# Optimization experiments

Measured on AMD Instinct MI355X. Metric: run time of the kernel, lower is better.

The kernel has to match this reference:

```python
import jax, jax.numpy as jnp
import numpy as np

# CIN config: input_dim (num_fields) = 32, cross_layer_sizes = [128, 128, 128], split_half = True
NUM_FIELDS = 32
EMBED_DIM = 16
BATCH = 4096
CROSS_SIZES = [128, 128, 128]


def setup_inputs() -> dict:
    key = jax.random.key(0)
    ks = jax.random.split(key, 8)
    x = jax.random.normal(ks[0], (BATCH, NUM_FIELDS, EMBED_DIM), dtype=jnp.float32)
    # Conv1d(kernel_size=1) weights: (out_ch, in_ch) + bias (out_ch,)
    prev = NUM_FIELDS
    inp = {"x": x}
    for i, cs in enumerate(CROSS_SIZES):
        in_ch = NUM_FIELDS * prev
        scale = 1.0 / np.sqrt(in_ch)
        inp[f"W{i}"] = jax.random.uniform(ks[1 + 2 * i], (cs, in_ch), dtype=jnp.float32, minval=-scale, maxval=scale)
        inp[f"b{i}"] = jax.random.uniform(ks[2 + 2 * i], (cs,), dtype=jnp.float32, minval=-scale, maxval=scale)
        prev = cs // 2  # split_half (applied after all but last, but prev for next conv uses halved size)
    return inp


def _cin_forward(x, Ws, bs):
    # x: (B, F, E)
    x0 = x
    h = x
    xs = []
    n_layers = len(Ws)
    for i in range(n_layers):
        B, F, E = x0.shape
        G = h.shape[1]
        # outer product over field dims -> (B, F*G, E)
        z = (x0[:, :, None, :] * h[:, None, :, :]).reshape(B, F * G, E)
        # 1x1 conv == channel matmul; bias broadcast over embed dim; relu
        y = jax.nn.relu(jnp.einsum('oc,bce->boe', Ws[i], z) + bs[i][None, :, None])
        if i != n_layers - 1:
            half = y.shape[1] // 2
            x_keep, h = y[:, :half, :], y[:, half:, :]
        else:
            x_keep, h = y, y
        xs.append(x_keep)
    return jnp.sum(jnp.concatenate(xs, axis=1), axis=2)  # (B, fc_input_dim)


def reference(x, W0, b0, W1, b1, W2, b2):
    return _cin_forward(x, [W0, W1, W2], [b0, b1, b2])
```

## Files before the change

kernel.cpp:

```cpp
#include <hip/hip_runtime.h>

typedef _Float16 half_t;
typedef _Float16 v8h __attribute__((ext_vector_type(8)));
typedef float v4f __attribute__((ext_vector_type(4)));

#define XTP 40

typedef __attribute__((address_space(3))) unsigned int lds_u32;
typedef const __attribute__((address_space(1))) unsigned int glb_u32;

__device__ __forceinline__ void dma16(const half_t* g, half_t* l, int lane) {
  __builtin_amdgcn_global_load_lds((glb_u32*)(g + lane * 8), (lds_u32*)(l), 16, 0, 0);
}

#define WAITVM(N) __builtin_amdgcn_s_waitcnt(0xF70 | (N))
#define SCHED0()  __builtin_amdgcn_sched_barrier(0)

__global__ __launch_bounds__(256) void prep_x(const float* __restrict__ x, half_t* __restrict__ xt) {
  __shared__ half_t t[8 * 512];
  const int tid = threadIdx.x;
  const size_t b0 = (size_t)blockIdx.x * 8;
#pragma unroll
  for (int i = 0; i < 4; ++i) {
    int idx = (i * 256 + tid) * 4;
    float4 v = *(const float4*)(x + b0 * 512 + idx);
    int e = idx & 15, f = (idx >> 4) & 31, b = idx >> 9;
    half_t* d = t + b * 512 + f;
    d[(e + 0) * 32] = (half_t)v.x;
    d[(e + 1) * 32] = (half_t)v.y;
    d[(e + 2) * 32] = (half_t)v.z;
    d[(e + 3) * 32] = (half_t)v.w;
  }
  __syncthreads();
#pragma unroll
  for (int i = 0; i < 2; ++i) {
    int c = i * 256 + tid;
    *(uint4*)(xt + b0 * 512 + c * 8) = *(const uint4*)(t + c * 8);
  }
}

__global__ __launch_bounds__(256) void prep_w(const float* __restrict__ src, half_t* __restrict__ dst,
                                              int ktot, int nchunk) {
  int i = blockIdx.x * 256 + threadIdx.x;
  if (i >= nchunk) return;
  int o = i & 127, k8 = i >> 7;
  const float* s = src + (size_t)o * ktot + k8 * 8;
  float4 f0 = *(const float4*)s;
  float4 f1 = *(const float4*)(s + 4);
  union { half_t h[8]; uint4 u; } pk;
  pk.h[0] = (half_t)f0.x; pk.h[1] = (half_t)f0.y; pk.h[2] = (half_t)f0.z; pk.h[3] = (half_t)f0.w;
  pk.h[4] = (half_t)f1.x; pk.h[5] = (half_t)f1.y; pk.h[6] = (half_t)f1.z; pk.h[7] = (half_t)f1.w;
  *(uint4*)(dst + (size_t)i * 8) = pk.u;
}

template <int G, int KTOT, int KEEP, int OUT_BASE, bool H_OUT, bool H_IS_X>
__global__ __launch_bounds__(512, 1) void cin_layer(const half_t* __restrict__ xt,
                                                    const half_t* __restrict__ hin,
                                                    const half_t* __restrict__ wgt,
                                                    const float* __restrict__ bias,
                                                    half_t* __restrict__ hout,
                                                    float* __restrict__ out) {
  constexpr int NS = KTOT / 32;
  constexpr int SPO = (G == 64) ? 16 : 8;
  constexpr int NOCT = NS / SPO;
  constexpr int NSEL = (G == 64) ? 2 : 1;
  __shared__ __align__(16) half_t xt_lds[256 * XTP];
  __shared__ __align__(16) half_t w_lds[4 * 4096];
  __shared__ float bias_lds[128];

  const int tid = threadIdx.x;
  const int lane = tid & 63;
  const int wv = tid >> 6;
  const size_t b0 = (size_t)blockIdx.x * 16;
  const int phase = (blockIdx.x >> 3) & 3;

  {
    const int r = tid >> 1, c = (tid & 1) * 16;
    const half_t* src = xt + b0 * 512 + r * 32 + c;
    uint4 q0 = *(const uint4*)(src);
    uint4 q1 = *(const uint4*)(src + 8);
    *(uint4*)(xt_lds + r * XTP + c) = q0;
    *(uint4*)(xt_lds + r * XTP + c + 8) = q1;
  }
  if (tid < 128) bias_lds[tid] = bias[tid];

  const int wm = (wv & 1) * 64;
  const int wb = (wv >> 1) * 4;
  const int col = lane & 15;
  const int kq = lane >> 4;

  int lrow[4];
#pragma unroll
  for (int ni = 0; ni < 4; ++ni) lrow[ni] = (wb + ni) * 16 + col;

  v8h hreg[4][NSEL];
  if (!H_IS_X) {
#pragma unroll
    for (int ni = 0; ni < 4; ++ni) {
      const half_t* hp = hin + ((b0 + wb + ni) * 16 + col) * 64 + kq * 8;
      hreg[ni][0] = *(const v8h*)(hp);
      if (NSEL > 1) hreg[ni][NSEL - 1] = *(const v8h*)(hp + 32);
    }
  }

#pragma unroll
  for (int p = 0; p < 3; ++p) {
    const half_t* wsrc = wgt + (size_t)(phase * SPO + p) * 4096;
    half_t* pb = w_lds + p * 4096;
    dma16(wsrc + wv * 512, pb + wv * 512, lane);
  }

  __syncthreads();

  if (H_IS_X) {
#pragma unroll
    for (int ni = 0; ni < 4; ++ni)
      hreg[ni][0] = *(const v8h*)(xt_lds + lrow[ni] * XTP + kq * 8);
  }

  v4f acc[4][4] = {};

#pragma unroll 1
  for (int oi = 0; oi < NOCT - 1; ++oi) {
    const int oct_a = (oi + phase) & 3;
    const int next_a = (oi + 1 + phase) & 3;
    v8h xv[4];
#pragma unroll
    for (int ni = 0; ni < 4; ++ni)
      xv[ni] = *(const v8h*)(xt_lds + lrow[ni] * XTP + oct_a * 8);
#pragma unroll
    for (int t = 0; t < SPO; ++t) {
      SCHED0(); WAITVM(2); __builtin_amdgcn_s_barrier(); SCHED0();
      {
        const int tp = t + 3;
        const half_t* wsrc = (tp < SPO)
            ? wgt + (size_t)(oct_a * SPO + tp) * 4096
            : wgt + (size_t)(next_a * SPO + (tp - SPO)) * 4096;
        half_t* pb = w_lds + (tp & 3) * 4096;
        dma16(wsrc + wv * 512, pb + wv * 512, lane);
      }
      const half_t* rb = w_lds + (t & 3) * 4096;
      const int j = (G == 64) ? (t >> 1) : t;
      const int sel = (G == 64) ? (t & 1) : 0;
      v8h a[4], bfr[4];
#pragma unroll
      for (int mi = 0; mi < 4; ++mi)
        a[mi] = *(const v8h*)(rb + (kq * 128 + wm + mi * 16 + col) * 8);
#pragma unroll
      for (int ni = 0; ni < 4; ++ni)
        bfr[ni] = hreg[ni][sel] * xv[ni][j];
#pragma unroll
      for (int mi = 0; mi < 4; ++mi)
#pragma unroll
        for (int ni = 0; ni < 4; ++ni)
          acc[mi][ni] = __builtin_amdgcn_mfma_f32_16x16x32_f16(a[mi], bfr[ni], acc[mi][ni], 0, 0, 0);
    }
  }

  {
    const int oct_a = (NOCT - 1 + phase) & 3;
    v8h xv[4];
#pragma unroll
    for (int ni = 0; ni < 4; ++ni)
      xv[ni] = *(const v8h*)(xt_lds + lrow[ni] * XTP + oct_a * 8);
#pragma unroll
    for (int t = 0; t < SPO; ++t) {
      SCHED0();
      if (t < SPO - 2) { WAITVM(2); } else if (t == SPO - 2) { WAITVM(1); } else { WAITVM(0); }
      __builtin_amdgcn_s_barrier(); SCHED0();
      if (t + 3 < SPO) {
        const int tp = t + 3;
        const half_t* wsrc = wgt + (size_t)(oct_a * SPO + tp) * 4096;
        half_t* pb = w_lds + (tp & 3) * 4096;
        dma16(wsrc + wv * 512, pb + wv * 512, lane);
      }
      const half_t* rb = w_lds + (t & 3) * 4096;
      const int j = (G == 64) ? (t >> 1) : t;
      const int sel = (G == 64) ? (t & 1) : 0;
      v8h a[4], bfr[4];
#pragma unroll
      for (int mi = 0; mi < 4; ++mi)
        a[mi] = *(const v8h*)(rb + (kq * 128 + wm + mi * 16 + col) * 8);
#pragma unroll
      for (int ni = 0; ni < 4; ++ni)
        bfr[ni] = hreg[ni][sel] * xv[ni][j];
#pragma unroll
      for (int mi = 0; mi < 4; ++mi)
#pragma unroll
        for (int ni = 0; ni < 4; ++ni)
          acc[mi][ni] = __builtin_amdgcn_mfma_f32_16x16x32_f16(a[mi], bfr[ni], acc[mi][ni], 0, 0, 0);
    }
  }

#pragma unroll
  for (int mi = 0; mi < 4; ++mi) {
    const int o_base = wm + mi * 16 + kq * 4;
#pragma unroll
    for (int ni = 0; ni < 4; ++ni) {
      const int bb = wb + ni;
      float v[4];
#pragma unroll
      for (int r = 0; r < 4; ++r)
        v[r] = fmaxf(acc[mi][ni][r] + bias_lds[o_base + r], 0.0f);
      if (H_OUT && o_base >= 64) {
        union { half_t h[4]; uint2 u; } pk;
#pragma unroll
        for (int r = 0; r < 4; ++r) pk.h[r] = (half_t)v[r];
        *(uint2*)(hout + ((b0 + bb) * 16 + col) * 64 + (o_base - 64)) = pk.u;
      }
      if (o_base < KEEP) {
#pragma unroll
        for (int r = 0; r < 4; ++r) {
          float sv = v[r];
          sv += __shfl_xor(sv, 1);
          sv += __shfl_xor(sv, 2);
          sv += __shfl_xor(sv, 4);
          sv += __shfl_xor(sv, 8);
          if (col == 0) out[(b0 + bb) * 256 + OUT_BASE + o_base + r] = sv;
        }
      }
    }
  }
}

extern "C" void kernel_launch(void* const* d_in, const int* in_sizes, int n_in,
                              void* d_out, int out_size, void* d_ws, size_t ws_size,
                              hipStream_t stream) {
  const float* x  = (const float*)d_in[0];
  const float* W0 = (const float*)d_in[1];
  const float* b0 = (const float*)d_in[2];
  const float* W1 = (const float*)d_in[3];
  const float* b1 = (const float*)d_in[4];
  const float* W2 = (const float*)d_in[5];
  const float* b2 = (const float*)d_in[6];
  float* out = (float*)d_out;
  char* ws = (char*)d_ws;

  half_t* xt  = (half_t*)(ws);
  half_t* w0h = (half_t*)(ws + (4u << 20));
  half_t* w1h = (half_t*)(ws + (4u << 20) + (256u << 10));
  half_t* w2h = (half_t*)(ws + (4u << 20) + (768u << 10));
  half_t* h1  = (half_t*)(ws + (4u << 20) + (1280u << 10));
  half_t* h2  = (half_t*)(ws + (12u << 20) + (1280u << 10));

  prep_x<<<512, 256, 0, stream>>>(x, xt);
  prep_w<<<64, 256, 0, stream>>>(W0, w0h, 1024, 16384);
  prep_w<<<128, 256, 0, stream>>>(W1, w1h, 2048, 32768);
  prep_w<<<128, 256, 0, stream>>>(W2, w2h, 2048, 32768);

  cin_layer<32, 1024, 64, 0, true, true><<<256, 512, 0, stream>>>(xt, xt, w0h, b0, h1, out);
  cin_layer<64, 2048, 64, 64, true, false><<<256, 512, 0, stream>>>(xt, h1, w1h, b1, h2, out);
  cin_layer<64, 2048, 128, 128, false, false><<<256, 512, 0, stream>>>(xt, h2, w2h, b2, nullptr, out);
}
```

Measured before the change: 178.5 us.

## Fuse input prep and all three CIN layers into one kernel with LDS-resident h

Replaces the separate prep_x kernel and three per-layer kernels with a single fused kernel. It converts x to fp16 directly into LDS, keeps the intermediate h activations in LDS between layers, and reads bias straight from global memory. The batch tile per block is halved to 8 rows with 512 blocks, and the three weight-conversion launches are merged into one. This removes the global round-trips for xt, h1 and h2 and several launches. In exchange, each block streams the full weight set, so total weight traffic doubles, and each barrier step now issues half as many MFMAs.

After: 148.7 us. 16.7% less time.

```diff
diff --git a/kernel.cpp b/kernel.cpp
--- a/kernel.cpp
+++ b/kernel.cpp
@@ -5,6 +5,7 @@
 typedef float v4f __attribute__((ext_vector_type(4)));
 
 #define XTP 40
+#define HP  72
 
 typedef __attribute__((address_space(3))) unsigned int lds_u32;
 typedef const __attribute__((address_space(1))) unsigned int glb_u32;
@@ -16,117 +17,77 @@
 #define WAITVM(N) __builtin_amdgcn_s_waitcnt(0xF70 | (N))
 #define SCHED0()  __builtin_amdgcn_sched_barrier(0)
 
-__global__ __launch_bounds__(256) void prep_x(const float* __restrict__ x, half_t* __restrict__ xt) {
-  __shared__ half_t t[8 * 512];
-  const int tid = threadIdx.x;
-  const size_t b0 = (size_t)blockIdx.x * 8;
-#pragma unroll
-  for (int i = 0; i < 4; ++i) {
-    int idx = (i * 256 + tid) * 4;
-    float4 v = *(const float4*)(x + b0 * 512 + idx);
-    int e = idx & 15, f = (idx >> 4) & 31, b = idx >> 9;
-    half_t* d = t + b * 512 + f;
-    d[(e + 0) * 32] = (half_t)v.x;
-    d[(e + 1) * 32] = (half_t)v.y;
-    d[(e + 2) * 32] = (half_t)v.z;
-    d[(e + 3) * 32] = (half_t)v.w;
-  }
-  __syncthreads();
-#pragma unroll
-  for (int i = 0; i < 2; ++i) {
-    int c = i * 256 + tid;
-    *(uint4*)(xt + b0 * 512 + c * 8) = *(const uint4*)(t + c * 8);
-  }
-}
-
-__global__ __launch_bounds__(256) void prep_w(const float* __restrict__ src, half_t* __restrict__ dst,
-                                              int ktot, int nchunk) {
+__global__ __launch_bounds__(256) void prep_w_all(const float* __restrict__ W0,
+                                                  const float* __restrict__ W1,
+                                                  const float* __restrict__ W2,
+                                                  half_t* __restrict__ w0h,
+                                                  half_t* __restrict__ w1h,
+                                                  half_t* __restrict__ w2h) {
   int i = blockIdx.x * 256 + threadIdx.x;
-  if (i >= nchunk) return;
-  int o = i & 127, k8 = i >> 7;
+  const float* src; half_t* dst; int ktot; int j;
+  if (i < 16384)      { src = W0; dst = w0h; ktot = 1024; j = i; }
+  else if (i < 49152) { src = W1; dst = w1h; ktot = 2048; j = i - 16384; }
+  else                { src = W2; dst = w2h; ktot = 2048; j = i - 49152; }
+  int o = j & 127, k8 = j >> 7;
   const float* s = src + (size_t)o * ktot + k8 * 8;
   float4 f0 = *(const float4*)s;
   float4 f1 = *(const float4*)(s + 4);
   union { half_t h[8]; uint4 u; } pk;
   pk.h[0] = (half_t)f0.x; pk.h[1] = (half_t)f0.y; pk.h[2] = (half_t)f0.z; pk.h[3] = (half_t)f0.w;
   pk.h[4] = (half_t)f1.x; pk.h[5] = (half_t)f1.y; pk.h[6] = (half_t)f1.z; pk.h[7] = (half_t)f1.w;
-  *(uint4*)(dst + (size_t)i * 8) = pk.u;
+  *(uint4*)(dst + (size_t)j * 8) = pk.u;
 }
 
 template <int G, int KTOT, int KEEP, int OUT_BASE, bool H_OUT, bool H_IS_X>
-__global__ __launch_bounds__(512, 1) void cin_layer(const half_t* __restrict__ xt,
-                                                    const half_t* __restrict__ hin,
-                                                    const half_t* __restrict__ wgt,
-                                                    const float* __restrict__ bias,
-                                                    half_t* __restrict__ hout,
-                                                    float* __restrict__ out) {
-  constexpr int NS = KTOT / 32;
+__device__ __forceinline__ void layer(const half_t* __restrict__ wgt,
+                                      const float* __restrict__ bias,
+                                      half_t* __restrict__ xt_lds,
+                                      half_t* __restrict__ h_lds,
+                                      half_t* __restrict__ w_ring,
+                                      float* __restrict__ out,
+                                      size_t b0, int tid, int phase) {
   constexpr int SPO = (G == 64) ? 16 : 8;
-  constexpr int NOCT = NS / SPO;
+  constexpr int NOCT = (KTOT / 32) / SPO;
   constexpr int NSEL = (G == 64) ? 2 : 1;
-  __shared__ __align__(16) half_t xt_lds[256 * XTP];
-  __shared__ __align__(16) half_t w_lds[4 * 4096];
-  __shared__ float bias_lds[128];
-
-  const int tid = threadIdx.x;
   const int lane = tid & 63;
   const int wv = tid >> 6;
-  const size_t b0 = (size_t)blockIdx.x * 16;
-  const int phase = (blockIdx.x >> 3) & 3;
-
-  {
-    const int r = tid >> 1, c = (tid & 1) * 16;
-    const half_t* src = xt + b0 * 512 + r * 32 + c;
-    uint4 q0 = *(const uint4*)(src);
-    uint4 q1 = *(const uint4*)(src + 8);
-    *(uint4*)(xt_lds + r * XTP + c) = q0;
-    *(uint4*)(xt_lds + r * XTP + c + 8) = q1;
-  }
-  if (tid < 128) bias_lds[tid] = bias[tid];
-
   const int wm = (wv & 1) * 64;
-  const int wb = (wv >> 1) * 4;
+  const int wb = (wv >> 1) * 2;
   const int col = lane & 15;
   const int kq = lane >> 4;
 
-  int lrow[4];
-#pragma unroll
-  for (int ni = 0; ni < 4; ++ni) lrow[ni] = (wb + ni) * 16 + col;
-
-  v8h hreg[4][NSEL];
-  if (!H_IS_X) {
-#pragma unroll
-    for (int ni = 0; ni < 4; ++ni) {
-      const half_t* hp = hin + ((b0 + wb + ni) * 16 + col) * 64 + kq * 8;
-      hreg[ni][0] = *(const v8h*)(hp);
-      if (NSEL > 1) hreg[ni][NSEL - 1] = *(const v8h*)(hp + 32);
-    }
+  int lrow[2];
+#pragma unroll
+  for (int ni = 0; ni < 2; ++ni) lrow[ni] = (wb + ni) * 16 + col;
+
+  __syncthreads();
+
+  const half_t* hb = H_IS_X ? xt_lds : h_lds;
+  const int hpitch = H_IS_X ? XTP : HP;
+  v8h hreg[2][NSEL];
+#pragma unroll
+  for (int ni = 0; ni < 2; ++ni) {
+    const half_t* hp = hb + lrow[ni] * hpitch + kq * 8;
+    hreg[ni][0] = *(const v8h*)hp;
+    if (NSEL > 1) hreg[ni][NSEL - 1] = *(const v8h*)(hp + 32);
   }
 
 #pragma unroll
   for (int p = 0; p < 3; ++p) {
     const half_t* wsrc = wgt + (size_t)(phase * SPO + p) * 4096;
-    half_t* pb = w_lds + p * 4096;
-    dma16(wsrc + wv * 512, pb + wv * 512, lane);
-  }
-
+    dma16(wsrc + wv * 512, w_ring + p * 4096 + wv * 512, lane);
+  }
   __syncthreads();
 
-  if (H_IS_X) {
-#pragma unroll
-    for (int ni = 0; ni < 4; ++ni)
-      hreg[ni][0] = *(const v8h*)(xt_lds + lrow[ni] * XTP + kq * 8);
-  }
-
-  v4f acc[4][4] = {};
+  v4f acc[4][2] = {};
 
 #pragma unroll 1
   for (int oi = 0; oi < NOCT - 1; ++oi) {
     const int oct_a = (oi + phase) & 3;
     const int next_a = (oi + 1 + phase) & 3;
-    v8h xv[4];
-#pragma unroll
-    for (int ni = 0; ni < 4; ++ni)
+    v8h xv[2];
+#pragma unroll
+    for (int ni = 0; ni < 2; ++ni)
       xv[ni] = *(const v8h*)(xt_lds + lrow[ni] * XTP + oct_a * 8);
 #pragma unroll
     for (int t = 0; t < SPO; ++t) {
@@ -136,32 +97,31 @@
         const half_t* wsrc = (tp < SPO)
             ? wgt + (size_t)(oct_a * SPO + tp) * 4096
             : wgt + (size_t)(next_a * SPO + (tp - SPO)) * 4096;
-        half_t* pb = w_lds + (tp & 3) * 4096;
-        dma16(wsrc + wv * 512, pb + wv * 512, lane);
-      }
-      const half_t* rb = w_lds + (t & 3) * 4096;
+        dma16(wsrc + wv * 512, w_ring + (tp & 3) * 4096 + wv * 512, lane);
+      }
+      const half_t* rb = w_ring + (t & 3) * 4096;
       const int j = (G == 64) ? (t >> 1) : t;
       const int sel = (G == 64) ? (t & 1) : 0;
-      v8h a[4], bfr[4];
+      v8h a[4], bfr[2];
 #pragma unroll
       for (int mi = 0; mi < 4; ++mi)
         a[mi] = *(const v8h*)(rb + (kq * 128 + wm + mi * 16 + col) * 8);
 #pragma unroll
-      for (int ni = 0; ni < 4; ++ni)
+      for (int ni = 0; ni < 2; ++ni)
         bfr[ni] = hreg[ni][sel] * xv[ni][j];
 #pragma unroll
       for (int mi = 0; mi < 4; ++mi)
 #pragma unroll
-        for (int ni = 0; ni < 4; ++ni)
+        for (int ni = 0; ni < 2; ++ni)
           acc[mi][ni] = __builtin_amdgcn_mfma_f32_16x16x32_f16(a[mi], bfr[ni], acc[mi][ni], 0, 0, 0);
     }
   }
 
   {
     const int oct_a = (NOCT - 1 + phase) & 3;
-    v8h xv[4];
-#pragma unroll
-    for (int ni = 0; ni < 4; ++ni)
+    v8h xv[2];
+#pragma unroll
+    for (int ni = 0; ni < 2; ++ni)
       xv[ni] = *(const v8h*)(xt_lds + lrow[ni] * XTP + oct_a * 8);
 #pragma unroll
     for (int t = 0; t < SPO; ++t) {
@@ -171,23 +131,22 @@
       if (t + 3 < SPO) {
         const int tp = t + 3;
         const half_t* wsrc = wgt + (size_t)(oct_a * SPO + tp) * 4096;
-        half_t* pb = w_lds + (tp & 3) * 4096;
-        dma16(wsrc + wv * 512, pb + wv * 512, lane);
-      }
-      const half_t* rb = w_lds + (t & 3) * 4096;
+        dma16(wsrc + wv * 512, w_ring + (tp & 3) * 4096 + wv * 512, lane);
+      }
+      const half_t* rb = w_ring + (t & 3) * 4096;
       const int j = (G == 64) ? (t >> 1) : t;
       const int sel = (G == 64) ? (t & 1) : 0;
-      v8h a[4], bfr[4];
+      v8h a[4], bfr[2];
 #pragma unroll
       for (int mi = 0; mi < 4; ++mi)
         a[mi] = *(const v8h*)(rb + (kq * 128 + wm + mi * 16 + col) * 8);
 #pragma unroll
-      for (int ni = 0; ni < 4; ++ni)
+      for (int ni = 0; ni < 2; ++ni)
         bfr[ni] = hreg[ni][sel] * xv[ni][j];
 #pragma unroll
       for (int mi = 0; mi < 4; ++mi)
 #pragma unroll
-        for (int ni = 0; ni < 4; ++ni)
+        for (int ni = 0; ni < 2; ++ni)
           acc[mi][ni] = __builtin_amdgcn_mfma_f32_16x16x32_f16(a[mi], bfr[ni], acc[mi][ni], 0, 0, 0);
     }
   }
@@ -195,18 +154,19 @@
 #pragma unroll
   for (int mi = 0; mi < 4; ++mi) {
     const int o_base = wm + mi * 16 + kq * 4;
-#pragma unroll
-    for (int ni = 0; ni < 4; ++ni) {
+    float4 b4 = *(const float4*)(bias + o_base);
+#pragma unroll
+    for (int ni = 0; ni < 2; ++ni) {
       const int bb = wb + ni;
       float v[4];
 #pragma unroll
       for (int r = 0; r < 4; ++r)
-        v[r] = fmaxf(acc[mi][ni][r] + bias_lds[o_base + r], 0.0f);
+        v[r] = fmaxf(acc[mi][ni][r] + (&b4.x)[r], 0.0f);
       if (H_OUT && o_base >= 64) {
         union { half_t h[4]; uint2 u; } pk;
 #pragma unroll
         for (int r = 0; r < 4; ++r) pk.h[r] = (half_t)v[r];
-        *(uint2*)(hout + ((b0 + bb) * 16 + col) * 64 + (o_base - 64)) = pk.u;
+        *(uint2*)(h_lds + (bb * 16 + col) * HP + (o_base - 64)) = pk.u;
       }
       if (o_base < KEEP) {
 #pragma unroll
@@ -221,6 +181,39 @@
       }
     }
   }
+}
+
+__global__ __launch_bounds__(512, 4) void cin_fused(const float* __restrict__ x,
+                                                    const half_t* __restrict__ w0h,
+                                                    const half_t* __restrict__ w1h,
+                                                    const half_t* __restrict__ w2h,
+                                                    const float* __restrict__ b0p,
+                                                    const float* __restrict__ b1p,
+                                                    const float* __restrict__ b2p,
+                                                    float* __restrict__ out) {
+  __shared__ __align__(16) half_t xt_lds[128 * XTP];
+  __shared__ __align__(16) half_t h_lds[128 * HP];
+  __shared__ __align__(16) half_t w_ring[4 * 4096];
+
+  const int tid = threadIdx.x;
+  const size_t b0 = (size_t)blockIdx.x * 8;
+  const int phase = (blockIdx.x >> 3) & 3;
+
+#pragma unroll
+  for (int i = 0; i < 2; ++i) {
+    int idx = (i * 512 + tid) * 4;
+    float4 v = *(const float4*)(x + b0 * 512 + idx);
+    int e = idx & 15, f = (idx >> 4) & 31, b = idx >> 9;
+    half_t* d = xt_lds + (b * 16 + e) * XTP + f;
+    d[0 * XTP] = (half_t)v.x;
+    d[1 * XTP] = (half_t)v.y;
+    d[2 * XTP] = (half_t)v.z;
+    d[3 * XTP] = (half_t)v.w;
+  }
+
+  layer<32, 1024, 64, 0, true, true>(w0h, b0p, xt_lds, h_lds, w_ring, out, b0, tid, phase);
+  layer<64, 2048, 64, 64, true, false>(w1h, b1p, xt_lds, h_lds, w_ring, out, b0, tid, phase);
+  layer<64, 2048, 128, 128, false, false>(w2h, b2p, xt_lds, h_lds, w_ring, out, b0, tid, phase);
 }
 
 extern "C" void kernel_launch(void* const* d_in, const int* in_sizes, int n_in,
@@ -236,19 +229,10 @@
   float* out = (float*)d_out;
   char* ws = (char*)d_ws;
 
-  half_t* xt  = (half_t*)(ws);
-  half_t* w0h = (half_t*)(ws + (4u << 20));
-  half_t* w1h = (half_t*)(ws + (4u << 20) + (256u << 10));
-  half_t* w2h = (half_t*)(ws + (4u << 20) + (768u << 10));
-  half_t* h1  = (half_t*)(ws + (4u << 20) + (1280u << 10));
-  half_t* h2  = (half_t*)(ws + (12u << 20) + (1280u << 10));
-
-  prep_x<<<512, 256, 0, stream>>>(x, xt);
-  prep_w<<<64, 256, 0, stream>>>(W0, w0h, 1024, 16384);
-  prep_w<<<128, 256, 0, stream>>>(W1, w1h, 2048, 32768);
-  prep_w<<<128, 256, 0, stream>>>(W2, w2h, 2048, 32768);
-
-  cin_layer<32, 1024, 64, 0, true, true><<<256, 512, 0, stream>>>(xt, xt, w0h, b0, h1, out);
-  cin_layer<64, 2048, 64, 64, true, false><<<256, 512, 0, stream>>>(xt, h1, w1h, b1, h2, out);
-  cin_layer<64, 2048, 128, 128, false, false><<<256, 512, 0, stream>>>(xt, h2, w2h, b2, nullptr, out);
-}
+  half_t* w0h = (half_t*)(ws);
+  half_t* w1h = (half_t*)(ws + (256u << 10));
+  half_t* w2h = (half_t*)(ws + (768u << 10));
+
+  prep_w_all<<<320, 256, 0, stream>>>(W0, W1, W2, w0h, w1h, w2h);
+  cin_fused<<<512, 512, 0, stream>>>(x, w0h, w1h, w2h, b0, b1, b2, out);
+}
```
